# Performance work log

Measured on AMD Instinct MI355X. Metric: run time of the kernel, lower is better.

## Reference

```python
import jax, jax.numpy as jnp
import numpy as np
from jax import lax


def _conv(x, w, b):
    # NCHW valid conv, stride 1 (torch Conv2d semantics)
    y = lax.conv_general_dilated(x, w, (1, 1), 'VALID',
                                 dimension_numbers=('NCHW', 'OIHW', 'NCHW'))
    return y + b[None, :, None, None]


def _maxpool(x, k, s):
    return lax.reduce_window(x, -jnp.inf, lax.max, (1, 1, k, k), (1, 1, s, s), 'VALID')


def _lin(x, w, b):
    # torch nn.Linear: y = x @ W^T + b, applied to last dim
    return x @ w.T + b


def setup_inputs() -> dict:
    key = jax.random.key(0)
    ks = jax.random.split(key, 21)
    def f(i, shape, scale):
        return jax.random.normal(ks[i], shape, dtype=jnp.float32) * scale
    return {
        'x': f(0, (512, 1, 28, 28), 1.0),
        'c1_w': f(1, (50, 1, 3, 3), 0.33), 'c1_b': f(2, (50,), 0.1),
        'c2_w': f(3, (50, 50, 3, 3), 0.047), 'c2_b': f(4, (50,), 0.05),
        'c3_w': f(5, (50, 50, 3, 3), 0.047), 'c3_b': f(6, (50,), 0.05),
        'l1_w': f(7, (500, 50), 0.14), 'l1_b': f(8, (500,), 0.05),
        'l2_w': f(9, (10, 500), 0.045), 'l2_b': f(10, (10,), 0.05),
        'd1_w': f(11, (3, 8450), 0.011), 'd1_b': f(12, (3,), 0.05),
        'd2_w': f(13, (2, 1250), 0.028), 'd2_b': f(14, (2,), 0.05),
        'c1c3_w': f(15, (13, 13), 0.28), 'c1c3_b': f(16, (13,), 0.05),
        'c1l1_w': f(17, (500, 1), 1.0), 'c1l1_b': f(18, (500,), 0.05),
        'c2l1_w': f(19, (500, 5), 0.45), 'c2l1_b': f(20, (500,), 0.05),
    }


def reference(x, c1_w, c1_b, c2_w, c2_b, c3_w, c3_b, l1_w, l1_b, l2_w, l2_b,
              d1_w, d1_b, d2_w, d2_b, c1c3_w, c1c3_b, c1l1_w, c1l1_b,
              c2l1_w, c2l1_b):
    B = x.shape[0]
    # stage 1: conv1 + relu + pool2 -> [B,50,13,13]
    h1 = _maxpool(jax.nn.relu(_conv(x, c1_w, c1_b)), 2, 2)
    # router 1 (argmax over 3 branches): 0 -> conv2 path, 1 -> c1_c3 path, 2 -> early-exit linear path
    d1 = jnp.argmax(_lin(h1.reshape(B, -1), d1_w, d1_b), axis=1)  # [B]
    # branch l11 (d1==2): pool7 -> [B,50,1,1], Linear(1->500) on last dim -> [B,50,1,500]
    l11 = _lin(_maxpool(h1, 7, 7), c1l1_w, c1l1_b)
    # branch c3-direct (d1==1): Linear(13->13) on last dim, then conv3+relu+pool2 -> [B,50,5,5]
    c33 = _lin(h1, c1c3_w, c1c3_b)
    c3d = _maxpool(jax.nn.relu(_conv(c33, c3_w, c3_b)), 2, 2)
    # branch c2 (d1==0): conv2+relu+pool2 -> [B,50,5,5]
    h2 = _maxpool(jax.nn.relu(_conv(h1, c2_w, c2_b)), 2, 2)
    # router 2 (argmax over 2 sub-branches)
    d2 = jnp.argmax(_lin(h2.reshape(B, -1), d2_w, d2_b), axis=1)  # [B]
    # sub-branch c32 (d2==0): conv3+relu+pool2 -> [B,50,1,1]
    c32 = _maxpool(jax.nn.relu(_conv(h2, c3_w, c3_b)), 2, 2)
    # sub-branch l12 (d2==1): Linear(5->500) on last dim -> [B,50,5,500], pool3 -> [B,50,1,166]
    l12 = _maxpool(_lin(h2, c2l1_w, c2l1_b), 3, 3)

    def head(t):
        # original: .view(-1, 50) -> linear1/relu/linear2/log_softmax; row-major flatten per sample
        r = t.reshape(B, -1, 50)
        return jax.nn.log_softmax(_lin(jax.nn.relu(_lin(r, l1_w, l1_b)), l2_w, l2_b), axis=-1)

    dt = x.dtype
    m_l11 = (d1 == 2).astype(dt)[:, None, None]
    m_c3d = (d1 == 1).astype(dt)[:, None, None]
    m_c32 = ((d1 == 0) & (d2 == 0)).astype(dt)[:, None, None]
    m_l12 = ((d1 == 0) & (d2 == 1)).astype(dt)[:, None, None]
    # dense masked combine (static-shape equivalent of the gather/compute/concat dispatch);
    # branch order matches the original concatenation: l11, l12, c32, c3-direct
    out = jnp.concatenate([head(l11) * m_l11, head(l12) * m_l12,
                           head(c32) * m_c32, head(c3d) * m_c3d], axis=1)  # [B,692,10]
    return out, d1, d2
```

## Files before the change

kernel.cpp:

```cpp
#include <hip/hip_runtime.h>
#include <hip/hip_bf16.h>
#include <math.h>

#define BB 512
#define CC 50

typedef __attribute__((ext_vector_type(8))) __bf16 bf16x8;
typedef __attribute__((ext_vector_type(4))) float f32x4;

__global__ void k_zero(float* __restrict__ out, int n4) {
  int i = blockIdx.x * 256 + threadIdx.x;
  if (i < n4) {
    float4 z = {0.f, 0.f, 0.f, 0.f};
    ((float4*)out)[i] = z;
  }
}

__global__ void k_pack(const float* __restrict__ l1w, const float* __restrict__ l1b,
                       const float* __restrict__ l2w,
                       __bf16* __restrict__ W1p, float* __restrict__ W2t) {
  int idx = blockIdx.x * 256 + threadIdx.x;
  if (idx < 512 * 64) {
    int j = idx >> 6, k = idx & 63;
    float v = 0.f;
    if (j < 500) {
      if (k < 50) v = l1w[j * 50 + k];
      else if (k == 50) v = l1b[j];
    }
    W1p[idx] = (__bf16)v;
  } else if (idx < 512 * 64 + 512 * 12) {
    int i2 = idx - 512 * 64;
    int j = i2 / 12, n = i2 % 12;
    W2t[i2] = (n < 10 && j < 500) ? l2w[n * 500 + j] : 0.f;
  }
}

__global__ void k_conv1(const float* __restrict__ x, const float* __restrict__ w,
                        const float* __restrict__ bias, float* __restrict__ h1) {
  int idx = blockIdx.x * 256 + threadIdx.x;
  if (idx >= BB * CC * 169) return;
  int b = idx / (CC * 169);
  int rem = idx % (CC * 169);
  int c = rem / 169;
  int p = rem % 169;
  int py = p / 13, px = p % 13;
  const float* xi = x + b * 784;
  float wr[9];
#pragma unroll
  for (int i = 0; i < 9; i++) wr[i] = w[c * 9 + i];
  float m = -INFINITY;
#pragma unroll
  for (int dy = 0; dy < 2; dy++)
#pragma unroll
    for (int dx = 0; dx < 2; dx++) {
      int y0 = 2 * py + dy, x0 = 2 * px + dx;
      float s = 0.f;
#pragma unroll
      for (int ky = 0; ky < 3; ky++)
#pragma unroll
        for (int kx = 0; kx < 3; kx++)
          s += xi[(y0 + ky) * 28 + x0 + kx] * wr[ky * 3 + kx];
      m = fmaxf(m, s);
    }
  h1[idx] = fmaxf(m + bias[c], 0.f);
}

__global__ void k_d1p7(const float* __restrict__ h1, const float* __restrict__ w,
                       const float* __restrict__ bias, int* __restrict__ d1i,
                       float* __restrict__ outd1, float* __restrict__ p7) {
  int b = blockIdx.x, t = threadIdx.x;
  const float* hb = h1 + b * 8450;
  float s0 = 0.f, s1 = 0.f, s2 = 0.f;
  for (int i = t; i < 8450; i += 256) {
    float v = hb[i];
    s0 += v * w[i];
    s1 += v * w[8450 + i];
    s2 += v * w[16900 + i];
  }
#pragma unroll
  for (int off = 32; off >= 1; off >>= 1) {
    s0 += __shfl_down(s0, off);
    s1 += __shfl_down(s1, off);
    s2 += __shfl_down(s2, off);
  }
  __shared__ float red[4][3];
  if ((t & 63) == 0) { red[t >> 6][0] = s0; red[t >> 6][1] = s1; red[t >> 6][2] = s2; }
  __syncthreads();
  if (t == 0) {
    float l0 = bias[0], l1v = bias[1], l2v = bias[2];
    for (int wv = 0; wv < 4; wv++) { l0 += red[wv][0]; l1v += red[wv][1]; l2v += red[wv][2]; }
    int idx = 0; float best = l0;
    if (l1v > best) { best = l1v; idx = 1; }
    if (l2v > best) { best = l2v; idx = 2; }
    d1i[b] = idx;
    outd1[b] = (float)idx;
  }
  if (t < 50) {
    const float* hp = hb + t * 169;
    float m = -INFINITY;
#pragma unroll
    for (int y = 0; y < 7; y++)
#pragma unroll
      for (int x = 0; x < 7; x++) m = fmaxf(m, hp[y * 13 + x]);
    p7[b * 50 + t] = m;
  }
}

template <int MODE>
__global__ __launch_bounds__(256) void k_conv5(const float* __restrict__ in,
                                               const float* __restrict__ w,
                                               const float* __restrict__ bias,
                                               const int* __restrict__ d1i,
                                               const float* __restrict__ w13,
                                               const float* __restrict__ b13,
                                               float* __restrict__ out) {
  int b = blockIdx.x;
  if (MODE == 1 && d1i[b] != 1) return;
  __shared__ float sh[50 * 260];
  __shared__ float w13s[182];
  int t = threadIdx.x;
  for (int i = t; i < 8450; i += 256) {
    int ic = i / 169, r = i % 169;
    int row = r / 13, xx = r % 13;
    sh[ic * 260 + row * 20 + xx] = in[b * 8450 + i];
  }
  if (MODE == 1) {
    for (int i = t; i < 182; i += 256) w13s[i] = (i < 169) ? w13[i] : b13[i - 169];
  }
  __syncthreads();
  if (MODE == 1) {
    for (int p = t; p < 650; p += 256) {
      float* row = sh + (p / 13) * 260 + (p % 13) * 20;
      float r[13];
#pragma unroll
      for (int k = 0; k < 13; k++) r[k] = row[k];
#pragma unroll
      for (int xx = 0; xx < 13; xx++) {
        float s = w13s[169 + xx];
#pragma unroll
        for (int k = 0; k < 13; k++) s += r[k] * w13s[xx * 13 + k];
        row[xx] = s;
      }
    }
    __syncthreads();
  }
  if (t >= 250) return;
  int oc = t / 5, py = t % 5;
  float acc[5][4];
#pragma unroll
  for (int i = 0; i < 5; i++)
#pragma unroll
    for (int j = 0; j < 4; j++) acc[i][j] = 0.f;
  const float* wb = w + oc * 450;
  for (int ic = 0; ic < 50; ic++) {
    float wv[9];
#pragma unroll
    for (int i = 0; i < 9; i++) wv[i] = wb[ic * 9 + i];
    float r[4][13];
    const float* rp = sh + ic * 260 + 2 * py * 20;
#pragma unroll
    for (int rr = 0; rr < 4; rr++) {
      const float* p4 = rp + rr * 20;
      float4 q0 = *(const float4*)(p4);
      float4 q1 = *(const float4*)(p4 + 4);
      float4 q2 = *(const float4*)(p4 + 8);
      r[rr][0] = q0.x; r[rr][1] = q0.y; r[rr][2] = q0.z; r[rr][3] = q0.w;
      r[rr][4] = q1.x; r[rr][5] = q1.y; r[rr][6] = q1.z; r[rr][7] = q1.w;
      r[rr][8] = q2.x; r[rr][9] = q2.y; r[rr][10] = q2.z; r[rr][11] = q2.w;
      r[rr][12] = p4[12];
    }
#pragma unroll
    for (int px = 0; px < 5; px++)
#pragma unroll
      for (int dy = 0; dy < 2; dy++)
#pragma unroll
        for (int dx = 0; dx < 2; dx++) {
          float s = acc[px][dy * 2 + dx];
          int x0 = 2 * px + dx;
#pragma unroll
          for (int ky = 0; ky < 3; ky++)
#pragma unroll
            for (int kx = 0; kx < 3; kx++)
              s += r[dy + ky][x0 + kx] * wv[ky * 3 + kx];
          acc[px][dy * 2 + dx] = s;
        }
  }
  float bs = bias[oc];
#pragma unroll
  for (int px = 0; px < 5; px++) {
    float m = fmaxf(fmaxf(acc[px][0], acc[px][1]), fmaxf(acc[px][2], acc[px][3]));
    out[((b * 50 + oc) * 5 + py) * 5 + px] = fmaxf(m + bs, 0.f);
  }
}

__global__ __launch_bounds__(256) void k_d2c(const float* __restrict__ h2,
                                             const float* __restrict__ d2w,
                                             const float* __restrict__ d2b,
                                             const float* __restrict__ c3w,
                                             const float* __restrict__ c3b,
                                             const float* __restrict__ c2l1w,
                                             const float* __restrict__ c2l1b,
                                             const int* __restrict__ d1i,
                                             int* __restrict__ d2i,
                                             float* __restrict__ outd2,
                                             float* __restrict__ c32,
                                             float* __restrict__ l12) {
  int b = blockIdx.x, t = threadIdx.x;
  __shared__ float hs[1250];
  __shared__ float wls[2500];
  __shared__ float bls[500];
  __shared__ float red[4][2];
  __shared__ int sd2;
  for (int i = t; i < 1250; i += 256) hs[i] = h2[b * 1250 + i];
  __syncthreads();
  float s0 = 0.f, s1 = 0.f;
  for (int i = t; i < 1250; i += 256) {
    float v = hs[i];
    s0 += v * d2w[i];
    s1 += v * d2w[1250 + i];
  }
#pragma unroll
  for (int off = 32; off >= 1; off >>= 1) {
    s0 += __shfl_down(s0, off);
    s1 += __shfl_down(s1, off);
  }
  if ((t & 63) == 0) { red[t >> 6][0] = s0; red[t >> 6][1] = s1; }
  __syncthreads();
  if (t == 0) {
    float l0 = d2b[0] + red[0][0] + red[1][0] + red[2][0] + red[3][0];
    float l1v = d2b[1] + red[0][1] + red[1][1] + red[2][1] + red[3][1];
    int idx = (l1v > l0) ? 1 : 0;
    d2i[b] = idx;
    outd2[b] = (float)idx;
    sd2 = idx;
  }
  __syncthreads();
  int d2v = sd2;
  if (d1i[b] != 0) return;
  if (d2v == 0) {
    if (t < 50) {
      const float* wb = c3w + t * 450;
      float a[4] = {0.f, 0.f, 0.f, 0.f};
      for (int ic = 0; ic < 50; ic++) {
        float r[4][4];
#pragma unroll
        for (int y = 0; y < 4; y++)
#pragma unroll
          for (int xx = 0; xx < 4; xx++) r[y][xx] = hs[ic * 25 + y * 5 + xx];
        float wv[9];
#pragma unroll
        for (int i = 0; i < 9; i++) wv[i] = wb[ic * 9 + i];
#pragma unroll
        for (int py = 0; py < 2; py++)
#pragma unroll
          for (int px = 0; px < 2; px++) {
            float s = a[py * 2 + px];
#pragma unroll
            for (int ky = 0; ky < 3; ky++)
#pragma unroll
              for (int kx = 0; kx < 3; kx++)
                s += r[py + ky][px + kx] * wv[ky * 3 + kx];
            a[py * 2 + px] = s;
          }
      }
      float m = fmaxf(fmaxf(a[0], a[1]), fmaxf(a[2], a[3]));
      c32[b * 50 + t] = fmaxf(m + c3b[t], 0.f);
    }
  } else {
    for (int i = t; i < 2500; i += 256) wls[i] = c2l1w[i];
    for (int i = t; i < 500; i += 256) bls[i] = c2l1b[i];
    __syncthreads();
    for (int o = t; o < 8300; o += 256) {
      int c = o / 166, tt = o % 166;
      const float* hb = hs + c * 25;
      float m = -INFINITY;
#pragma unroll
      for (int i = 0; i < 3; i++) {
        float a0 = hb[i * 5 + 0], a1 = hb[i * 5 + 1], a2 = hb[i * 5 + 2],
              a3 = hb[i * 5 + 3], a4 = hb[i * 5 + 4];
#pragma unroll
        for (int dj = 0; dj < 3; dj++) {
          int j = 3 * tt + dj;
          const float* wj = wls + j * 5;
          float s = bls[j] + a0 * wj[0] + a1 * wj[1] + a2 * wj[2] + a3 * wj[3] + a4 * wj[4];
          m = fmaxf(m, s);
        }
      }
      l12[b * 8300 + o] = m;
    }
  }
}

__global__ void k_count(const int* __restrict__ d1i, const int* __restrict__ d2i,
                        int* __restrict__ off, int* __restrict__ ntot) {
  __shared__ int s[512];
  int t = threadIdx.x;
  int d1 = d1i[t], d2 = d2i[t];
  int nr = (d1 == 2) ? 500 : (d1 == 1) ? 25 : (d2 == 1) ? 166 : 1;
  s[t] = nr;
  __syncthreads();
  for (int o = 1; o < 512; o <<= 1) {
    int v = (t >= o) ? s[t - o] : 0;
    __syncthreads();
    s[t] += v;
    __syncthreads();
  }
  off[t] = s[t] - nr;
  if (t == 511) ntot[0] = s[511];
}

__global__ void k_fill(const int* __restrict__ d1i, const int* __restrict__ d2i,
                       const int* __restrict__ off, int* __restrict__ rowtab) {
  int b = blockIdx.x;
  int d1 = d1i[b], d2 = d2i[b];
  int nr, rstart;
  if (d1 == 2)      { nr = 500; rstart = 0; }
  else if (d1 == 1) { nr = 25;  rstart = 667; }
  else if (d2 == 1) { nr = 166; rstart = 500; }
  else              { nr = 1;   rstart = 666; }
  int o = off[b];
  for (int i = threadIdx.x; i < nr; i += 256)
    rowtab[o + i] = (b << 10) | (rstart + i);
}

__device__ __forceinline__ int swz(int byteoff) {
  return byteoff ^ (((byteoff >> 7) & 7) << 4);
}

__global__ __launch_bounds__(256, 3) void k_headc(
    const float* __restrict__ c3d, const float* __restrict__ c32,
    const float* __restrict__ p7, const float* __restrict__ l12buf,
    const int* __restrict__ rowtab, const int* __restrict__ ntotp,
    const __bf16* __restrict__ W1p, const float* __restrict__ W2t,
    const float* __restrict__ l2b,
    const float* __restrict__ c1l1w, const float* __restrict__ c1l1b,
    float* __restrict__ out) {
  int ntot = ntotp[0];
  int blkbase = blockIdx.x * 64;
  if (blkbase >= ntot) return;

  __shared__ __align__(16) char wlds[16384];
  __shared__ __align__(16) float w2s[512 * 12];
  int t = threadIdx.x;
  int wv = t >> 6, lane = t & 63;
  int lr = lane & 15, lg = lane >> 4;

  for (int i = t; i < 1536; i += 256)
    ((float4*)w2s)[i] = ((const float4*)W2t)[i];

  int row = blkbase + wv * 16 + lr;
  int rowc = (row < ntot) ? row : (ntot - 1);
  int e = rowtab[rowc];
  int gb = e >> 10, orow = e & 1023;
  bf16x8 a1[2];
  {
    float pv = 0.f;
    const float* wsrc = nullptr;
    const float* bsrc = nullptr;
    const float* src = nullptr;
    bool isl11 = (orow < 500);
    if (isl11) {
      pv = p7[gb * 50 + orow / 10];
      int q = (orow % 10) * 50;
      wsrc = c1l1w + q;
      bsrc = c1l1b + q;
    } else if (orow < 666) {
      src = l12buf + gb * 8300 + (orow - 500) * 50;
    } else if (orow == 666) {
      src = c32 + gb * 50;
    } else {
      src = c3d + gb * 1250 + (orow - 667) * 50;
    }
#pragma unroll
    for (int ks = 0; ks < 2; ++ks) {
      float v[8];
      int k0 = ks * 32 + lg * 8;
      if (ks == 0 || lg < 2) {
        if (isl11) {
#pragma unroll
          for (int i = 0; i < 8; i += 2) {
            float2 wq = *(const float2*)(wsrc + k0 + i);
            float2 bq = *(const float2*)(bsrc + k0 + i);
            v[i] = pv * wq.x + bq.x;
            v[i + 1] = pv * wq.y + bq.y;
          }
        } else {
#pragma unroll
          for (int i = 0; i < 8; i += 2) {
            float2 q = *(const float2*)(src + k0 + i);
            v[i] = q.x; v[i + 1] = q.y;
          }
        }
      } else if (lg == 2) {
        float2 q;
        if (isl11) {
          float2 wq = *(const float2*)(wsrc + 48);
          float2 bq = *(const float2*)(bsrc + 48);
          q.x = pv * wq.x + bq.x; q.y = pv * wq.y + bq.y;
        } else {
          q = *(const float2*)(src + 48);
        }
        v[0] = q.x; v[1] = q.y; v[2] = 1.0f;
        v[3] = 0.f; v[4] = 0.f; v[5] = 0.f; v[6] = 0.f; v[7] = 0.f;
      } else {
#pragma unroll
        for (int i = 0; i < 8; ++i) v[i] = 0.f;
      }
      bf16x8 a;
#pragma unroll
      for (int i = 0; i < 8; ++i) a[i] = (__bf16)v[i];
      a1[ks] = a;
    }
  }

  float acc[4][10];
#pragma unroll
  for (int r = 0; r < 4; ++r)
#pragma unroll
    for (int n = 0; n < 10; ++n) acc[r][n] = 0.f;

  for (int p = 0; p < 4; ++p) {
    if (p > 0) __syncthreads();
    {
      const char* src = (const char*)W1p + p * 16384 + t * 64;
#pragma unroll
      for (int i = 0; i < 4; ++i) {
        float4 q = *(const float4*)(src + i * 16);
        *(float4*)(wlds + swz(t * 64 + i * 16)) = q;
      }
    }
    __syncthreads();
#pragma unroll
    for (int jl = 0; jl < 8; ++jl) {
      int jt = p * 8 + jl;
      int boff = jl * 2048 + lr * 128 + lg * 16;
      bf16x8 b0 = *(const bf16x8*)(wlds + swz(boff));
      bf16x8 b1 = *(const bf16x8*)(wlds + swz(boff + 64));
      const float* wr = w2s + (jt * 16 + lr) * 12;
      float4 w20 = *(const float4*)(wr);
      float4 w21 = *(const float4*)(wr + 4);
      float2 w22 = *(const float2*)(wr + 8);
      f32x4 h = {0.f, 0.f, 0.f, 0.f};
      h = __builtin_amdgcn_mfma_f32_16x16x32_bf16(a1[0], b0, h, 0, 0, 0);
      h = __builtin_amdgcn_mfma_f32_16x16x32_bf16(a1[1], b1, h, 0, 0, 0);
      float w2v[10] = {w20.x, w20.y, w20.z, w20.w, w21.x, w21.y, w21.z, w21.w, w22.x, w22.y};
#pragma unroll
      for (int r = 0; r < 4; ++r) {
        float hv = fmaxf(h[r], 0.f);
#pragma unroll
        for (int n = 0; n < 10; ++n) acc[r][n] += hv * w2v[n];
      }
    }
  }

#pragma unroll
  for (int r = 0; r < 4; ++r)
#pragma unroll
    for (int n = 0; n < 10; ++n) {
      float v = acc[r][n];
      v += __shfl_xor(v, 1);
      v += __shfl_xor(v, 2);
      v += __shfl_xor(v, 4);
      v += __shfl_xor(v, 8);
      acc[r][n] = v;
    }
  if (lr == 0) {
#pragma unroll
    for (int r = 0; r < 4; ++r) {
      int rw = blkbase + wv * 16 + lg * 4 + r;
      if (rw < ntot) {
        int e2 = rowtab[rw];
        int b2 = e2 >> 10, orow2 = e2 & 1023;
        float o[10];
        float m = -INFINITY;
#pragma unroll
        for (int n = 0; n < 10; ++n) {
          o[n] = acc[r][n] + l2b[n];
          m = fmaxf(m, o[n]);
        }
        float s = 0.f;
#pragma unroll
        for (int n = 0; n < 10; ++n) s += expf(o[n] - m);
        float lse = m + logf(s);
        float* orowp = out + (b2 * 692 + orow2) * 10;
#pragma unroll
        for (int n = 0; n < 10; ++n) orowp[n] = o[n] - lse;
      }
    }
  }
}

extern "C" void kernel_launch(void* const* d_in, const int* in_sizes, int n_in,
                              void* d_out, int out_size, void* d_ws, size_t ws_size,
                              hipStream_t stream) {
  const float* x     = (const float*)d_in[0];
  const float* c1w   = (const float*)d_in[1];
  const float* c1b   = (const float*)d_in[2];
  const float* c2w   = (const float*)d_in[3];
  const float* c2b   = (const float*)d_in[4];
  const float* c3w   = (const float*)d_in[5];
  const float* c3b   = (const float*)d_in[6];
  const float* l1w   = (const float*)d_in[7];
  const float* l1b   = (const float*)d_in[8];
  const float* l2w   = (const float*)d_in[9];
  const float* l2b   = (const float*)d_in[10];
  const float* d1w   = (const float*)d_in[11];
  const float* d1b   = (const float*)d_in[12];
  const float* d2w   = (const float*)d_in[13];
  const float* d2b   = (const float*)d_in[14];
  const float* c13w  = (const float*)d_in[15];
  const float* c13b  = (const float*)d_in[16];
  const float* c1l1w = (const float*)d_in[17];
  const float* c1l1b = (const float*)d_in[18];
  const float* c2l1w = (const float*)d_in[19];
  const float* c2l1b = (const float*)d_in[20];
  float* out = (float*)d_out;

  float* ws  = (float*)d_ws;
  float* h1  = ws;
  float* h2  = h1 + 4326400;
  float* c3d = h2 + 640000;
  float* c32 = c3d + 640000;
  float* p7  = c32 + 25600;
  int*   d1i = (int*)(p7 + 25600);
  int*   d2i = d1i + 512;
  __bf16* W1p = (__bf16*)(d2i + 512);
  float* W2t = (float*)(W1p + 512 * 64);
  int* off    = (int*)(W2t + 512 * 12);
  int* ntot   = off + 512;
  int* rowtab = ntot + 4;
  float* l12buf = h1;

  float* outd1 = out + 512 * 692 * 10;
  float* outd2 = outd1 + 512;

  k_zero<<<3460, 256, 0, stream>>>(out, 885510);
  k_pack<<<153, 256, 0, stream>>>(l1w, l1b, l2w, W1p, W2t);
  k_conv1<<<16900, 256, 0, stream>>>(x, c1w, c1b, h1);
  k_d1p7<<<512, 256, 0, stream>>>(h1, d1w, d1b, d1i, outd1, p7);
  k_conv5<0><<<512, 256, 0, stream>>>(h1, c2w, c2b, d1i, c13w, c13b, h2);
  k_conv5<1><<<512, 256, 0, stream>>>(h1, c3w, c3b, d1i, c13w, c13b, c3d);
  k_d2c<<<512, 256, 0, stream>>>(h2, d2w, d2b, c3w, c3b, c2l1w, c2l1b,
                                 d1i, d2i, outd2, c32, l12buf);
  k_count<<<1, 512, 0, stream>>>(d1i, d2i, off, ntot);
  k_fill<<<512, 256, 0, stream>>>(d1i, d2i, off, rowtab);
  k_headc<<<4000, 256, 0, stream>>>(c3d, c32, p7, l12buf, rowtab, ntot,
                                    W1p, W2t, l2b, c1l1w, c1l1b, out);
}
```

Measured before the change: 222.0 us.

## Merge conv2 and c3-direct conv kernels and split pool rows across threads

The two conv5 launches (conv2 path and the c1c3/conv3 direct path) become a single launch with 1024 blocks of 512 threads. Even blocks do conv2 and odd blocks do the c3-direct path. Each thread now computes one of the two pooling rows (dy) and keeps half as many accumulators, with the 2x2 max finished through a lane shuffle. This aims to double thread-level parallelism, cut per-thread register pressure and drop one launch, at the cost of re-reading overlapping input rows from shared memory and running a runtime mode branch.

```diff
diff --git a/kernel.cpp b/kernel.cpp
--- a/kernel.cpp
+++ b/kernel.cpp
@@ -106,30 +106,29 @@
   }
 }
 
-template <int MODE>
-__global__ __launch_bounds__(256) void k_conv5(const float* __restrict__ in,
-                                               const float* __restrict__ w,
-                                               const float* __restrict__ bias,
-                                               const int* __restrict__ d1i,
-                                               const float* __restrict__ w13,
-                                               const float* __restrict__ b13,
-                                               float* __restrict__ out) {
-  int b = blockIdx.x;
-  if (MODE == 1 && d1i[b] != 1) return;
+__global__ __launch_bounds__(512) void k_conv5m(
+    const float* __restrict__ h1,
+    const float* __restrict__ c2w, const float* __restrict__ c2b,
+    const float* __restrict__ c3w, const float* __restrict__ c3b,
+    const int* __restrict__ d1i,
+    const float* __restrict__ w13, const float* __restrict__ b13,
+    float* __restrict__ h2, float* __restrict__ c3d) {
+  int id = blockIdx.x;
+  int mode = id & 1, b = id >> 1;
+  if (mode == 1 && d1i[b] != 1) return;
   __shared__ float sh[50 * 260];
   __shared__ float w13s[182];
   int t = threadIdx.x;
-  for (int i = t; i < 8450; i += 256) {
+  for (int i = t; i < 8450; i += 512) {
     int ic = i / 169, r = i % 169;
-    int row = r / 13, xx = r % 13;
-    sh[ic * 260 + row * 20 + xx] = in[b * 8450 + i];
-  }
-  if (MODE == 1) {
-    for (int i = t; i < 182; i += 256) w13s[i] = (i < 169) ? w13[i] : b13[i - 169];
+    sh[ic * 260 + (r / 13) * 20 + (r % 13)] = h1[b * 8450 + i];
+  }
+  if (mode == 1) {
+    for (int i = t; i < 182; i += 512) w13s[i] = (i < 169) ? w13[i] : b13[i - 169];
   }
   __syncthreads();
-  if (MODE == 1) {
-    for (int p = t; p < 650; p += 256) {
+  if (mode == 1) {
+    for (int p = t; p < 650; p += 512) {
       float* row = sh + (p / 13) * 260 + (p % 13) * 20;
       float r[13];
 #pragma unroll
@@ -144,22 +143,20 @@
     }
     __syncthreads();
   }
-  if (t >= 250) return;
-  int oc = t / 5, py = t % 5;
-  float acc[5][4];
-#pragma unroll
-  for (int i = 0; i < 5; i++)
-#pragma unroll
-    for (int j = 0; j < 4; j++) acc[i][j] = 0.f;
-  const float* wb = w + oc * 450;
+  if (t >= 500) return;
+  int oc = t / 10, rem = t % 10, py = rem >> 1, dy = rem & 1;
+  const float* wb = (mode ? c3w : c2w) + oc * 450;
+  float acc[5][2];
+#pragma unroll
+  for (int i = 0; i < 5; i++) { acc[i][0] = 0.f; acc[i][1] = 0.f; }
   for (int ic = 0; ic < 50; ic++) {
     float wv[9];
 #pragma unroll
     for (int i = 0; i < 9; i++) wv[i] = wb[ic * 9 + i];
-    float r[4][13];
-    const float* rp = sh + ic * 260 + 2 * py * 20;
-#pragma unroll
-    for (int rr = 0; rr < 4; rr++) {
+    float r[3][13];
+    const float* rp = sh + ic * 260 + (2 * py + dy) * 20;
+#pragma unroll
+    for (int rr = 0; rr < 3; rr++) {
       const float* p4 = rp + rr * 20;
       float4 q0 = *(const float4*)(p4);
       float4 q1 = *(const float4*)(p4 + 4);
@@ -172,24 +169,26 @@
 #pragma unroll
     for (int px = 0; px < 5; px++)
 #pragma unroll
-      for (int dy = 0; dy < 2; dy++)
-#pragma unroll
-        for (int dx = 0; dx < 2; dx++) {
-          float s = acc[px][dy * 2 + dx];
-          int x0 = 2 * px + dx;
-#pragma unroll
-          for (int ky = 0; ky < 3; ky++)
-#pragma unroll
-            for (int kx = 0; kx < 3; kx++)
-              s += r[dy + ky][x0 + kx] * wv[ky * 3 + kx];
-          acc[px][dy * 2 + dx] = s;
-        }
-  }
-  float bs = bias[oc];
+      for (int dx = 0; dx < 2; dx++) {
+        float s = acc[px][dx];
+        int x0 = 2 * px + dx;
+#pragma unroll
+        for (int ky = 0; ky < 3; ky++)
+#pragma unroll
+          for (int kx = 0; kx < 3; kx++)
+            s += r[ky][x0 + kx] * wv[ky * 3 + kx];
+        acc[px][dx] = s;
+      }
+  }
+  float bs = (mode ? c3b : c2b)[oc];
+  float* outp = mode ? c3d : h2;
 #pragma unroll
   for (int px = 0; px < 5; px++) {
-    float m = fmaxf(fmaxf(acc[px][0], acc[px][1]), fmaxf(acc[px][2], acc[px][3]));
-    out[((b * 50 + oc) * 5 + py) * 5 + px] = fmaxf(m + bs, 0.f);
+    float m = fmaxf(acc[px][0], acc[px][1]);
+    float mo = __shfl_xor(m, 1);
+    m = fmaxf(m, mo);
+    if (dy == 0)
+      outp[(b * 50 + oc) * 25 + py * 5 + px] = fmaxf(m + bs, 0.f);
   }
 }
 
@@ -538,8 +537,8 @@
   k_pack<<<153, 256, 0, stream>>>(l1w, l1b, l2w, W1p, W2t);
   k_conv1<<<16900, 256, 0, stream>>>(x, c1w, c1b, h1);
   k_d1p7<<<512, 256, 0, stream>>>(h1, d1w, d1b, d1i, outd1, p7);
-  k_conv5<0><<<512, 256, 0, stream>>>(h1, c2w, c2b, d1i, c13w, c13b, h2);
-  k_conv5<1><<<512, 256, 0, stream>>>(h1, c3w, c3b, d1i, c13w, c13b, c3d);
+  k_conv5m<<<1024, 512, 0, stream>>>(h1, c2w, c2b, c3w, c3b, d1i,
+                                     c13w, c13b, h2, c3d);
   k_d2c<<<512, 256, 0, stream>>>(h2, d2w, d2b, c3w, c3b, c2l1w, c2l1b,
                                  d1i, d2i, outd2, c32, l12buf);
   k_count<<<1, 512, 0, stream>>>(d1i, d2i, off, ntot);
```

Result: slower. 261.9 us (+18.0%).
